# Kernel optimization log

Measured on AMD Instinct MI355X. Metric: run time of the kernel, lower is better.

## Reference

```python
import jax, jax.numpy as jnp
import numpy as np

D_MODEL = 1024
D_FF = 4096
N_HEADS = 16
D_HEAD = D_MODEL // N_HEADS
BSZ, SEQ = 2, 2048
EPS = 1e-6


def layer_norm(x, lam, beta):
    # torch impl: (x - mu) / (std_biased + eps) * lambda + beta
    mu = jnp.mean(x, axis=-1, keepdims=True)
    sigma = jnp.sqrt(jnp.mean((x - mu) ** 2, axis=-1, keepdims=True)) + EPS
    return (x - mu) / sigma * lam + beta


def setup_inputs() -> dict:
    key = jax.random.key(0)
    ks = jax.random.split(key, 10)
    s = 0.02
    x = jax.random.normal(ks[0], (BSZ, SEQ, D_MODEL), dtype=jnp.float32)
    mask = jnp.ones((BSZ, 1, 1, SEQ), dtype=jnp.int32)
    # nn.Linear weights stored [out, in]; y = x @ W.T
    Wq = jax.random.normal(ks[1], (D_MODEL, D_MODEL), dtype=jnp.float32) * s
    Wk = jax.random.normal(ks[2], (D_MODEL, D_MODEL), dtype=jnp.float32) * s
    Wv = jax.random.normal(ks[3], (D_MODEL, D_MODEL), dtype=jnp.float32) * s
    Wo = jax.random.normal(ks[4], (D_MODEL, D_MODEL), dtype=jnp.float32) * s
    w1 = jax.random.normal(ks[5], (D_FF, D_MODEL), dtype=jnp.float32) * s
    b1 = jnp.zeros((D_FF,), dtype=jnp.float32)
    w2 = jax.random.normal(ks[6], (D_MODEL, D_FF), dtype=jnp.float32) * s
    b2 = jnp.zeros((D_MODEL,), dtype=jnp.float32)
    g1 = jnp.ones((D_MODEL,), dtype=jnp.float32)
    be1 = jnp.zeros((D_MODEL,), dtype=jnp.float32)
    g2 = jnp.ones((D_MODEL,), dtype=jnp.float32)
    be2 = jnp.zeros((D_MODEL,), dtype=jnp.float32)
    return {"x": x, "mask": mask, "Wq": Wq, "Wk": Wk, "Wv": Wv, "Wo": Wo,
            "w1": w1, "b1": b1, "w2": w2, "b2": b2,
            "g1": g1, "be1": be1, "g2": g2, "be2": be2}


def reference(x, mask, Wq, Wk, Wv, Wo, w1, b1, w2, b2, g1, be1, g2, be2):
    b, s, _ = x.shape
    # projections (y = x @ W.T), split heads -> [b, h, s, dh]
    def split_heads(t):
        return t.reshape(b, s, N_HEADS, D_HEAD).transpose(0, 2, 1, 3)
    Q = split_heads(x @ Wq.T)
    K = split_heads(x @ Wk.T)
    V = split_heads(x @ Wv.T)
    score = jnp.einsum('bhqd,bhkd->bhqk', Q, K) / jnp.sqrt(jnp.float32(D_HEAD))
    score = jnp.where(mask == 0, -jnp.inf, score)
    attn = jax.nn.softmax(score, axis=-1)
    out = jnp.einsum('bhqk,bhkd->bhqd', attn, V)
    out = out.transpose(0, 2, 1, 3).reshape(b, s, D_MODEL)
    x1 = out @ Wo.T
    x2 = layer_norm(x1 + x, g1, be1)
    x3 = jax.nn.relu(x2 @ w1.T + b1) @ w2.T + b2
    x4 = layer_norm(x2 + x3, g2, be2)
    return x4
```

## Files before the change

kernel.cpp:

```cpp
#include <hip/hip_runtime.h>
#include <math.h>

typedef __attribute__((ext_vector_type(8))) short bf16x8;
typedef __attribute__((ext_vector_type(4))) float f32x4;
typedef __attribute__((ext_vector_type(8))) unsigned short us8;
typedef unsigned short u16;
typedef unsigned int u32;

constexpr int BSZ = 2, SEQ = 2048, DM = 1024, DFF = 4096, NH = 16, DH = 64;
constexpr int MROWS = BSZ * SEQ;

__device__ __forceinline__ float bf2f(u16 u) {
  union { unsigned int i; float f; } v; v.i = ((unsigned int)u) << 16; return v.f;
}
__device__ __forceinline__ u16 f2bf(float f) {
  union { float f; unsigned int i; } v; v.f = f;
  unsigned int r = v.i + 0x7fffu + ((v.i >> 16) & 1u);
  return (u16)(r >> 16);
}

#define GLOAD16(gp, lp) __builtin_amdgcn_global_load_lds( \
    (const __attribute__((address_space(1))) void*)(gp),  \
    (__attribute__((address_space(3))) void*)(lp), 16, 0, 0)
#define GLOAD4(gp, lp) __builtin_amdgcn_global_load_lds( \
    (const __attribute__((address_space(1))) void*)(gp),  \
    (__attribute__((address_space(3))) void*)(lp), 4, 0, 0)

__global__ __launch_bounds__(256) void cvt_all(
    const float* __restrict__ x, const float* __restrict__ Wq,
    const float* __restrict__ Wk, const float* __restrict__ Wv,
    const float* __restrict__ Wo, const float* __restrict__ w1,
    const float* __restrict__ w2, u16* __restrict__ xb,
    u16* __restrict__ Wqkvb, u16* __restrict__ Wob,
    u16* __restrict__ w1b, u16* __restrict__ w2b) {
  constexpr int M1 = 1 << 20;
  const int i = (blockIdx.x * 256 + threadIdx.x) * 8;
  const float* src;
  u16* dst;
  int off;
  if (i < 4 * M1)        { src = x;  dst = xb;            off = i;           }
  else if (i < 5 * M1)   { src = Wq; dst = Wqkvb;         off = i - 4 * M1;  }
  else if (i < 6 * M1)   { src = Wk; dst = Wqkvb + M1;    off = i - 5 * M1;  }
  else if (i < 7 * M1)   { src = Wv; dst = Wqkvb + 2 * M1; off = i - 6 * M1; }
  else if (i < 8 * M1)   { src = Wo; dst = Wob;           off = i - 7 * M1;  }
  else if (i < 12 * M1)  { src = w1; dst = w1b;           off = i - 8 * M1;  }
  else                   { src = w2; dst = w2b;           off = i - 12 * M1; }
  const float4 a = *(const float4*)(src + off);
  const float4 b = *(const float4*)(src + off + 4);
  uint4 o;
  o.x = f2bf(a.x) | ((unsigned)f2bf(a.y) << 16);
  o.y = f2bf(a.z) | ((unsigned)f2bf(a.w) << 16);
  o.z = f2bf(b.x) | ((unsigned)f2bf(b.y) << 16);
  o.w = f2bf(b.z) | ((unsigned)f2bf(b.w) << 16);
  *(uint4*)(dst + off) = o;
}

template <int BM, int BN, bool BIAS, bool RELU, bool OBF16>
__global__ __launch_bounds__(256) void gemm_bf16(
    const u16* __restrict__ A, const u16* __restrict__ B,
    const float* __restrict__ bias, float* __restrict__ Cf,
    u16* __restrict__ Cb, int M, int N, int K) {
  constexpr int MI = BM / 32, NI = BN / 32;
  __shared__ u16 As[2][BM * 32];
  __shared__ u16 Bs[2][BN * 32];
  const int tid = threadIdx.x;
  const int lane = tid & 63, wid = tid >> 6;

  const int nwg = gridDim.x * gridDim.y;
  int id = blockIdx.y * gridDim.x + blockIdx.x;
  id = (id & 7) * (nwg >> 3) + (id >> 3);
  const int bx = id % gridDim.x, by = id / gridDim.x;

  const int row0 = by * BM, col0 = bx * BN;
  const int wr = (wid >> 1) * (BM / 2), wc = (wid & 1) * (BN / 2);
  const int fr = lane & 15, hi = lane >> 4;

  f32x4 acc[MI][NI];
#pragma unroll
  for (int i = 0; i < MI; ++i)
#pragma unroll
    for (int j = 0; j < NI; ++j) acc[i][j] = {0.f, 0.f, 0.f, 0.f};

  const int sr = tid >> 2;
  const int se = (tid & 3) * 8;

#define STAGE(buf, k0)                                                        \
  {                                                                           \
    _Pragma("unroll")                                                         \
    for (int c = 0; c < BM * 64; c += 4096) {                                 \
      const int r = (c >> 6) + sr;                                            \
      GLOAD16(A + (size_t)(row0 + r) * K + ((k0) + se),                       \
              ((char*)As[buf]) + c + tid * 16);                               \
    }                                                                         \
    _Pragma("unroll")                                                         \
    for (int c = 0; c < BN * 64; c += 4096) {                                 \
      const int r = (c >> 6) + sr;                                            \
      GLOAD16(B + (size_t)(col0 + r) * K + ((k0) + se),                       \
              ((char*)Bs[buf]) + c + tid * 16);                               \
    }                                                                         \
  }

  STAGE(0, 0);
  __syncthreads();

  const int NIT = K / 32;
  for (int it = 0; it < NIT; ++it) {
    const int cur = it & 1;
    if (it + 1 < NIT) STAGE(cur ^ 1, (it + 1) * 32);

    bf16x8 af[MI], bv[NI];
#pragma unroll
    for (int mi = 0; mi < MI; ++mi)
      af[mi] = *(const bf16x8*)&As[cur][(wr + mi * 16 + fr) * 32 + hi * 8];
#pragma unroll
    for (int ni = 0; ni < NI; ++ni)
      bv[ni] = *(const bf16x8*)&Bs[cur][(wc + ni * 16 + fr) * 32 + hi * 8];
#pragma unroll
    for (int mi = 0; mi < MI; ++mi)
#pragma unroll
      for (int ni = 0; ni < NI; ++ni)
        acc[mi][ni] = __builtin_amdgcn_mfma_f32_16x16x32_bf16(
            af[mi], bv[ni], acc[mi][ni], 0, 0, 0);
    __syncthreads();
  }
#undef STAGE

  const int erow = row0 + wr + (hi << 2);
  const int ecol0 = col0 + wc;
#pragma unroll
  for (int ni = 0; ni < NI; ++ni) {
    const int col = ecol0 + ni * 16 + fr;
    const float bvv = BIAS ? bias[col] : 0.f;
#pragma unroll
    for (int mi = 0; mi < MI; ++mi) {
      const int rbase = erow + mi * 16;
#pragma unroll
      for (int j = 0; j < 4; ++j) {
        float v = acc[mi][ni][j] + bvv;
        if (RELU) v = fmaxf(v, 0.f);
        const size_t idx = (size_t)(rbase + j) * N + col;
        if (OBF16) Cb[idx] = f2bf(v); else Cf[idx] = v;
      }
    }
  }
}

__global__ __launch_bounds__(512) void attn_mfma(
    const u16* __restrict__ QKV, const int* __restrict__ mask,
    u16* __restrict__ Ob) {
  constexpr int KB = 64, QB = 128, NT = SEQ / KB;
  __shared__ u16 Kl[2][KB * 64];
  __shared__ u16 Vt[2][64 * KB];
  __shared__ int ml[2][KB];

  const int tid = threadIdx.x;
  const int lane = tid & 63, wid = tid >> 6;
  const int q0 = blockIdx.x * QB;
  const int bh = blockIdx.y;
  const int b = bh >> 4, h = bh & 15;
  const size_t base = (size_t)b * SEQ * 3072;
  const int fr = lane & 15, g = lane >> 4;

  const u16* qp = QKV + base + (size_t)(q0 + wid * 16 + fr) * 3072 + h * 64 + g * 8;
  bf16x8 qf0, qf1;
  {
    const float QSC = 0.18033688f;
    const us8 ua = *(const us8*)qp;
    const us8 ub = *(const us8*)(qp + 32);
    u32 pa[4], pb[4];
#pragma unroll
    for (int i = 0; i < 4; ++i) {
      const float a0 = bf2f(ua[2 * i]) * QSC, a1 = bf2f(ua[2 * i + 1]) * QSC;
      const float b0 = bf2f(ub[2 * i]) * QSC, b1 = bf2f(ub[2 * i + 1]) * QSC;
      asm("v_cvt_pk_bf16_f32 %0, %1, %2" : "=v"(pa[i]) : "v"(a0), "v"(a1));
      asm("v_cvt_pk_bf16_f32 %0, %1, %2" : "=v"(pb[i]) : "v"(b0), "v"(b1));
    }
    union { u32 d[4]; bf16x8 v; } c0, c1;
#pragma unroll
    for (int i = 0; i < 4; ++i) { c0.d[i] = pa[i]; c1.d[i] = pb[i]; }
    qf0 = c0.v; qf1 = c1.v;
  }

  const int krow = wid * 8 + (lane >> 3);
  const int kcol = 8 * ((lane & 7) ^ (lane >> 3));
  const u16* ksrc = QKV + base + 1024 + h * 64 + kcol;
  const int kdst = wid * 1024 + lane * 16;

  const int va = (tid & 255) >> 3;
  const int vq = tid & 7;
  const u16* vsrc = QKV + base + 2048 + h * 64 + vq * 8;
  const bool vstage = (wid < 4);

  f32x4 o[4] = {{0.f,0.f,0.f,0.f},{0.f,0.f,0.f,0.f},{0.f,0.f,0.f,0.f},{0.f,0.f,0.f,0.f}};
  float mreg = -3e38f, lreg = 0.f;

  {
    GLOAD16(ksrc + (size_t)krow * 3072, (char*)Kl[0] + kdst);
    if (wid == 4) GLOAD4(mask + b * SEQ + lane, (char*)ml[0] + lane * 4);
    if (vstage) {
      const us8 v0 = *(const us8*)(vsrc + (size_t)(2 * va) * 3072);
      const us8 v1 = *(const us8*)(vsrc + (size_t)(2 * va + 1) * 3072);
      char* vb = (char*)Vt[0];
#pragma unroll
      for (int i = 0; i < 8; ++i) {
        const int d = vq * 8 + i;
        const u32 wv = (u32)(u16)v0[i] | ((u32)(u16)v1[i] << 16);
        *(u32*)(vb + d * 128 + ((4 * va) ^ ((vq ^ i) << 4))) = wv;
      }
    }
  }
  __syncthreads();

  for (int it = 0; it < NT; ++it) {
    const int cur = it & 1, nxt = cur ^ 1;
    const int ktn = (it + 1) * KB;
    const bool pre = (it + 1 < NT);
    us8 v0 = {}, v1 = {};
    if (pre) {
      GLOAD16(ksrc + (size_t)(ktn + krow) * 3072, (char*)Kl[nxt] + kdst);
      if (wid == 4) GLOAD4(mask + b * SEQ + ktn + lane, (char*)ml[nxt] + lane * 4);
      if (vstage) {
        v0 = *(const us8*)(vsrc + (size_t)(ktn + 2 * va) * 3072);
        v1 = *(const us8*)(vsrc + (size_t)(ktn + 2 * va + 1) * 3072);
      }
    }

    f32x4 s[4];
#pragma unroll
    for (int t16 = 0; t16 < 4; ++t16) {
      const int kr = t16 * 16 + fr;
      const char* krp = (const char*)Kl[cur] + kr * 128;
      const int sw = (kr & 7) << 4;
      const bf16x8 kf0 = *(const bf16x8*)(krp + ((g * 16) ^ sw));
      const bf16x8 kf1 = *(const bf16x8*)(krp + ((g * 16 + 64) ^ sw));
      f32x4 a = {0.f, 0.f, 0.f, 0.f};
      a = __builtin_amdgcn_mfma_f32_16x16x32_bf16(kf0, qf0, a, 0, 0, 0);
      a = __builtin_amdgcn_mfma_f32_16x16x32_bf16(kf1, qf1, a, 0, 0, 0);
      s[t16] = a;
    }

#pragma unroll
    for (int t16 = 0; t16 < 4; ++t16) {
      const int4 mv = *(const int4*)&ml[cur][t16 * 16 + g * 4];
      const int* mp = (const int*)&mv;
#pragma unroll
      for (int j = 0; j < 4; ++j)
        if (mp[j] == 0) s[t16][j] = -3e38f;
    }

    float rmax = s[0][0];
#pragma unroll
    for (int t16 = 0; t16 < 4; ++t16)
#pragma unroll
      for (int j = 0; j < 4; ++j) rmax = fmaxf(rmax, s[t16][j]);

    if (!__all(rmax <= mreg + 12.f)) {
      rmax = fmaxf(rmax, __shfl_xor(rmax, 16));
      rmax = fmaxf(rmax, __shfl_xor(rmax, 32));
      const float mn = fmaxf(mreg, rmax);
      float sc;
      asm("v_exp_f32 %0, %1" : "=v"(sc) : "v"(mreg - mn));
      mreg = mn;
      lreg *= sc;
#pragma unroll
      for (int j = 0; j < 4; ++j) {
        const float scj = __shfl(sc, (g << 4) + g * 4 + j);
#pragma unroll
        for (int dt = 0; dt < 4; ++dt) o[dt][j] *= scj;
      }
    }

    float p[4][4];
#pragma unroll
    for (int t16 = 0; t16 < 4; ++t16)
#pragma unroll
      for (int j = 0; j < 4; ++j) {
        float e;
        asm("v_exp_f32 %0, %1" : "=v"(e) : "v"(s[t16][j] - mreg));
        p[t16][j] = e;
        lreg += e;
      }

    u32 plo[4], phi[4];
#pragma unroll
    for (int t16 = 0; t16 < 4; ++t16) {
      asm("v_cvt_pk_bf16_f32 %0, %1, %2"
          : "=v"(plo[t16]) : "v"(p[t16][0]), "v"(p[t16][1]));
      asm("v_cvt_pk_bf16_f32 %0, %1, %2"
          : "=v"(phi[t16]) : "v"(p[t16][2]), "v"(p[t16][3]));
    }

#pragma unroll
    for (int kh = 0; kh < 2; ++kh) {
      u32 fd[4];
#pragma unroll
      for (int hf = 0; hf < 2; ++hf) {
        const int sl = fr + ((((g & 1) << 1) + hf) << 4);
        const u32 c0l = (u32)__shfl((int)plo[kh * 2], sl);
        const u32 c0h = (u32)__shfl((int)phi[kh * 2], sl);
        const u32 c1l = (u32)__shfl((int)plo[kh * 2 + 1], sl);
        const u32 c1h = (u32)__shfl((int)phi[kh * 2 + 1], sl);
        const bool s1 = ((g >> 1) & 1) != 0;
        fd[hf * 2] = s1 ? c1l : c0l;
        fd[hf * 2 + 1] = s1 ? c1h : c0h;
      }
      union { u32 d[4]; bf16x8 v; } uu;
      uu.d[0] = fd[0]; uu.d[1] = fd[1]; uu.d[2] = fd[2]; uu.d[3] = fd[3];
      const bf16x8 pf = uu.v;
#pragma unroll
      for (int dt = 0; dt < 4; ++dt) {
        const int d = dt * 16 + fr;
        const int xd = (((d >> 3) ^ d) & 7) << 4;
        const bf16x8 vf = *(const bf16x8*)((const char*)Vt[cur] + d * 128 +
                                           ((g * 16 + kh * 64) ^ xd));
        o[dt] = __builtin_amdgcn_mfma_f32_16x16x32_bf16(pf, vf, o[dt], 0, 0, 0);
      }
    }

    if (pre && vstage) {
      char* vb = (char*)Vt[nxt];
#pragma unroll
      for (int i = 0; i < 8; ++i) {
        const int d = vq * 8 + i;
        const u32 wv = (u32)(u16)v0[i] | ((u32)(u16)v1[i] << 16);
        *(u32*)(vb + d * 128 + ((4 * va) ^ ((vq ^ i) << 4))) = wv;
      }
    }
    __syncthreads();
  }

  lreg += __shfl_xor(lreg, 16);
  lreg += __shfl_xor(lreg, 32);
  const float inv = 1.f / lreg;
#pragma unroll
  for (int j = 0; j < 4; ++j) {
    const float invj = __shfl(inv, (g << 4) + g * 4 + j);
    const int qrow = q0 + wid * 16 + g * 4 + j;
    u16* orow = Ob + (size_t)(b * SEQ + qrow) * DM + h * 64;
#pragma unroll
    for (int dt = 0; dt < 4; ++dt)
      orow[dt * 16 + fr] = f2bf(o[dt][j] * invj);
  }
}

template <bool ABF, bool BBF, bool OBF>
__global__ __launch_bounds__(256) void ln_add(const void* __restrict__ Ap,
                                              const void* __restrict__ Bp,
                                              const float* __restrict__ g,
                                              const float* __restrict__ be,
                                              void* __restrict__ outp) {
  __shared__ float red[2][4];
  __shared__ float mu_s, sig_s;
  const int row = blockIdx.x;
  const int tid = threadIdx.x;

  float4 a, b;
  if (ABF) {
    const ushort4 u = *(const ushort4*)((const u16*)Ap + (size_t)row * DM + tid * 4);
    a = make_float4(bf2f(u.x), bf2f(u.y), bf2f(u.z), bf2f(u.w));
  } else {
    a = *(const float4*)((const float*)Ap + (size_t)row * DM + tid * 4);
  }
  if (BBF) {
    const ushort4 u = *(const ushort4*)((const u16*)Bp + (size_t)row * DM + tid * 4);
    b = make_float4(bf2f(u.x), bf2f(u.y), bf2f(u.z), bf2f(u.w));
  } else {
    b = *(const float4*)((const float*)Bp + (size_t)row * DM + tid * 4);
  }
  float4 s = make_float4(a.x + b.x, a.y + b.y, a.z + b.z, a.w + b.w);

  float sum = s.x + s.y + s.z + s.w;
  float sq = s.x * s.x + s.y * s.y + s.z * s.z + s.w * s.w;
#pragma unroll
  for (int off = 32; off >= 1; off >>= 1) {
    sum += __shfl_xor(sum, off);
    sq += __shfl_xor(sq, off);
  }
  const int wid = tid >> 6;
  if ((tid & 63) == 0) { red[0][wid] = sum; red[1][wid] = sq; }
  __syncthreads();
  if (tid == 0) {
    float ts = red[0][0] + red[0][1] + red[0][2] + red[0][3];
    float tq = red[1][0] + red[1][1] + red[1][2] + red[1][3];
    float mu = ts * (1.f / DM);
    float var = tq * (1.f / DM) - mu * mu;
    mu_s = mu;
    sig_s = sqrtf(fmaxf(var, 0.f)) + 1e-6f;
  }
  __syncthreads();
  const float mu = mu_s, inv = 1.f / sig_s;
  const float4 gv = *(const float4*)(g + tid * 4);
  const float4 bv = *(const float4*)(be + tid * 4);
  float4 o;
  o.x = (s.x - mu) * inv * gv.x + bv.x;
  o.y = (s.y - mu) * inv * gv.y + bv.y;
  o.z = (s.z - mu) * inv * gv.z + bv.z;
  o.w = (s.w - mu) * inv * gv.w + bv.w;
  if (OBF) {
    u16* op = (u16*)outp + (size_t)row * DM + tid * 4;
    ushort4 o4;
    o4.x = f2bf(o.x); o4.y = f2bf(o.y); o4.z = f2bf(o.z); o4.w = f2bf(o.w);
    *(ushort4*)op = o4;
  } else {
    *(float4*)((float*)outp + (size_t)row * DM + tid * 4) = o;
  }
}

extern "C" void kernel_launch(void* const* d_in, const int* in_sizes, int n_in,
                              void* d_out, int out_size, void* d_ws,
                              size_t ws_size, hipStream_t stream) {
  const float* x  = (const float*)d_in[0];
  const int* mask = (const int*)d_in[1];
  const float* Wq = (const float*)d_in[2];
  const float* Wk = (const float*)d_in[3];
  const float* Wv = (const float*)d_in[4];
  const float* Wo = (const float*)d_in[5];
  const float* w1 = (const float*)d_in[6];
  const float* b1 = (const float*)d_in[7];
  const float* w2 = (const float*)d_in[8];
  const float* b2 = (const float*)d_in[9];
  const float* g1 = (const float*)d_in[10];
  const float* be1 = (const float*)d_in[11];
  const float* g2 = (const float*)d_in[12];
  const float* be2 = (const float*)d_in[13];
  float* out = (float*)d_out;
  float* ws = (float*)d_ws;

  u16*   QKVb  = (u16*)(ws + 0);
  u16*   xb    = (u16*)(ws + 6291456);
  u16*   Wqkvb = (u16*)(ws + 8388608);
  u16*   Wob   = (u16*)(ws + 9961472);
  u16*   w1b   = (u16*)(ws + 10485760);
  u16*   w2b   = (u16*)(ws + 12582912);
  u16*   Obf   = (u16*)(ws + 14680064);
  u16*   X1b   = (u16*)(ws + 16777216);
  u16*   X2b   = (u16*)(ws + 20971520);
  u16*   X3b   = (u16*)(ws + 23068672);
  u16*   Hb    = (u16*)(ws + 0);

  const dim3 blk(256);

  cvt_all<<<8192, blk, 0, stream>>>(x, Wq, Wk, Wv, Wo, w1, w2,
                                    xb, Wqkvb, Wob, w1b, w2b);

  gemm_bf16<128, 128, false, false, true><<<dim3(3072 / 128, MROWS / 128), blk, 0, stream>>>(
      xb, Wqkvb, nullptr, nullptr, QKVb, MROWS, 3072, DM);

  attn_mfma<<<dim3(SEQ / 128, BSZ * NH), dim3(512), 0, stream>>>(QKVb, mask, Obf);

  gemm_bf16<64, 128, false, false, true><<<dim3(DM / 128, MROWS / 64), blk, 0, stream>>>(
      Obf, Wob, nullptr, nullptr, X1b, MROWS, DM, DM);

  ln_add<true, true, true><<<dim3(MROWS), blk, 0, stream>>>(X1b, xb, g1, be1, X2b);

  gemm_bf16<128, 128, true, true, true><<<dim3(DFF / 128, MROWS / 128), blk, 0, stream>>>(
      X2b, w1b, b1, nullptr, Hb, MROWS, DFF, DM);

  gemm_bf16<64, 128, true, false, true><<<dim3(DM / 128, MROWS / 64), blk, 0, stream>>>(
      Hb, w2b, b2, nullptr, X3b, MROWS, DM, DFF);

  ln_add<true, true, false><<<dim3(MROWS), blk, 0, stream>>>(X2b, X3b, g2, be2, out);
}
```

Measured before the change: 272.3 us.

## Split-K the Wo and W2 GEMMs into two halves, summed in layernorm

```diff
diff --git a/kernel.cpp b/kernel.cpp
--- a/kernel.cpp
+++ b/kernel.cpp
@@ -55,11 +55,11 @@
   *(uint4*)(dst + off) = o;
 }
 
-template <int BM, int BN, bool BIAS, bool RELU, bool OBF16>
+template <int BM, int BN, bool BIAS, bool RELU>
 __global__ __launch_bounds__(256) void gemm_bf16(
     const u16* __restrict__ A, const u16* __restrict__ B,
-    const float* __restrict__ bias, float* __restrict__ Cf,
-    u16* __restrict__ Cb, int M, int N, int K) {
+    const float* __restrict__ bias, u16* __restrict__ Cb,
+    int M, int N, int K, int ld) {
   constexpr int MI = BM / 32, NI = BN / 32;
   __shared__ u16 As[2][BM * 32];
   __shared__ u16 Bs[2][BN * 32];
@@ -71,6 +71,10 @@
   id = (id & 7) * (nwg >> 3) + (id >> 3);
   const int bx = id % gridDim.x, by = id / gridDim.x;
 
+  const u16* Az = A + (size_t)blockIdx.z * K;
+  const u16* Bz = B + (size_t)blockIdx.z * K;
+  u16* Cz = Cb + (size_t)blockIdx.z * M * N;
+
   const int row0 = by * BM, col0 = bx * BN;
   const int wr = (wid >> 1) * (BM / 2), wc = (wid & 1) * (BN / 2);
   const int fr = lane & 15, hi = lane >> 4;
@@ -89,13 +93,13 @@
     _Pragma("unroll")                                                         \
     for (int c = 0; c < BM * 64; c += 4096) {                                 \
       const int r = (c >> 6) + sr;                                            \
-      GLOAD16(A + (size_t)(row0 + r) * K + ((k0) + se),                       \
+      GLOAD16(Az + (size_t)(row0 + r) * ld + ((k0) + se),                     \
               ((char*)As[buf]) + c + tid * 16);                               \
     }                                                                         \
     _Pragma("unroll")                                                         \
     for (int c = 0; c < BN * 64; c += 4096) {                                 \
       const int r = (c >> 6) + sr;                                            \
-      GLOAD16(B + (size_t)(col0 + r) * K + ((k0) + se),                       \
+      GLOAD16(Bz + (size_t)(col0 + r) * ld + ((k0) + se),                     \
               ((char*)Bs[buf]) + c + tid * 16);                               \
     }                                                                         \
   }
@@ -138,8 +142,7 @@
       for (int j = 0; j < 4; ++j) {
         float v = acc[mi][ni][j] + bvv;
         if (RELU) v = fmaxf(v, 0.f);
-        const size_t idx = (size_t)(rbase + j) * N + col;
-        if (OBF16) Cb[idx] = f2bf(v); else Cf[idx] = v;
+        Cz[(size_t)(rbase + j) * N + col] = f2bf(v);
       }
     }
   }
@@ -343,38 +346,37 @@
   }
 }
 
-template <bool ABF, bool BBF, bool OBF>
-__global__ __launch_bounds__(256) void ln_add(const void* __restrict__ Ap,
-                                              const void* __restrict__ Bp,
-                                              const float* __restrict__ g,
-                                              const float* __restrict__ be,
-                                              void* __restrict__ outp) {
+template <bool OBF, bool HASC, bool HASB>
+__global__ __launch_bounds__(256) void ln_add(
+    const u16* __restrict__ Ap, const u16* __restrict__ Bp,
+    const u16* __restrict__ Cp, const float* __restrict__ bias,
+    const float* __restrict__ g, const float* __restrict__ be,
+    void* __restrict__ outp) {
   __shared__ float red[2][4];
   __shared__ float mu_s, sig_s;
   const int row = blockIdx.x;
   const int tid = threadIdx.x;
-
-  float4 a, b;
-  if (ABF) {
-    const ushort4 u = *(const ushort4*)((const u16*)Ap + (size_t)row * DM + tid * 4);
-    a = make_float4(bf2f(u.x), bf2f(u.y), bf2f(u.z), bf2f(u.w));
-  } else {
-    a = *(const float4*)((const float*)Ap + (size_t)row * DM + tid * 4);
-  }
-  if (BBF) {
-    const ushort4 u = *(const ushort4*)((const u16*)Bp + (size_t)row * DM + tid * 4);
-    b = make_float4(bf2f(u.x), bf2f(u.y), bf2f(u.z), bf2f(u.w));
-  } else {
-    b = *(const float4*)((const float*)Bp + (size_t)row * DM + tid * 4);
-  }
-  float4 s = make_float4(a.x + b.x, a.y + b.y, a.z + b.z, a.w + b.w);
+  const size_t off = (size_t)row * DM + tid * 4;
+
+  const ushort4 ua = *(const ushort4*)(Ap + off);
+  const ushort4 ub = *(const ushort4*)(Bp + off);
+  float4 s = make_float4(bf2f(ua.x) + bf2f(ub.x), bf2f(ua.y) + bf2f(ub.y),
+                         bf2f(ua.z) + bf2f(ub.z), bf2f(ua.w) + bf2f(ub.w));
+  if (HASC) {
+    const ushort4 uc = *(const ushort4*)(Cp + off);
+    s.x += bf2f(uc.x); s.y += bf2f(uc.y); s.z += bf2f(uc.z); s.w += bf2f(uc.w);
+  }
+  if (HASB) {
+    const float4 bb = *(const float4*)(bias + tid * 4);
+    s.x += bb.x; s.y += bb.y; s.z += bb.z; s.w += bb.w;
+  }
 
   float sum = s.x + s.y + s.z + s.w;
   float sq = s.x * s.x + s.y * s.y + s.z * s.z + s.w * s.w;
 #pragma unroll
-  for (int off = 32; off >= 1; off >>= 1) {
-    sum += __shfl_xor(sum, off);
-    sq += __shfl_xor(sq, off);
+  for (int off2 = 32; off2 >= 1; off2 >>= 1) {
+    sum += __shfl_xor(sum, off2);
+    sq += __shfl_xor(sq, off2);
   }
   const int wid = tid >> 6;
   if ((tid & 63) == 0) { red[0][wid] = sum; red[1][wid] = sq; }
@@ -397,12 +399,12 @@
   o.z = (s.z - mu) * inv * gv.z + bv.z;
   o.w = (s.w - mu) * inv * gv.w + bv.w;
   if (OBF) {
-    u16* op = (u16*)outp + (size_t)row * DM + tid * 4;
+    u16* op = (u16*)outp + off;
     ushort4 o4;
     o4.x = f2bf(o.x); o4.y = f2bf(o.y); o4.z = f2bf(o.z); o4.w = f2bf(o.w);
     *(ushort4*)op = o4;
   } else {
-    *(float4*)((float*)outp + (size_t)row * DM + tid * 4) = o;
+    *(float4*)((float*)outp + off) = o;
   }
 }
 
@@ -433,9 +435,11 @@
   u16*   w1b   = (u16*)(ws + 10485760);
   u16*   w2b   = (u16*)(ws + 12582912);
   u16*   Obf   = (u16*)(ws + 14680064);
-  u16*   X1b   = (u16*)(ws + 16777216);
+  u16*   X1a   = (u16*)(ws + 16777216);
+  u16*   X1c   = (u16*)(ws + 18874368);
   u16*   X2b   = (u16*)(ws + 20971520);
-  u16*   X3b   = (u16*)(ws + 23068672);
+  u16*   X3a   = (u16*)(ws + 23068672);
+  u16*   X3c   = (u16*)(ws + 25165824);
   u16*   Hb    = (u16*)(ws + 0);
 
   const dim3 blk(256);
@@ -443,21 +447,23 @@
   cvt_all<<<8192, blk, 0, stream>>>(x, Wq, Wk, Wv, Wo, w1, w2,
                                     xb, Wqkvb, Wob, w1b, w2b);
 
-  gemm_bf16<128, 128, false, false, true><<<dim3(3072 / 128, MROWS / 128), blk, 0, stream>>>(
-      xb, Wqkvb, nullptr, nullptr, QKVb, MROWS, 3072, DM);
+  gemm_bf16<128, 128, false, false><<<dim3(3072 / 128, MROWS / 128), blk, 0, stream>>>(
+      xb, Wqkvb, nullptr, QKVb, MROWS, 3072, DM, DM);
 
   attn_mfma<<<dim3(SEQ / 128, BSZ * NH), dim3(512), 0, stream>>>(QKVb, mask, Obf);
 
-  gemm_bf16<64, 128, false, false, true><<<dim3(DM / 128, MROWS / 64), blk, 0, stream>>>(
-      Obf, Wob, nullptr, nullptr, X1b, MROWS, DM, DM);
-
-  ln_add<true, true, true><<<dim3(MROWS), blk, 0, stream>>>(X1b, xb, g1, be1, X2b);
-
-  gemm_bf16<128, 128, true, true, true><<<dim3(DFF / 128, MROWS / 128), blk, 0, stream>>>(
-      X2b, w1b, b1, nullptr, Hb, MROWS, DFF, DM);
-
-  gemm_bf16<64, 128, true, false, true><<<dim3(DM / 128, MROWS / 64), blk, 0, stream>>>(
-      Hb, w2b, b2, nullptr, X3b, MROWS, DM, DFF);
-
-  ln_add<true, true, false><<<dim3(MROWS), blk, 0, stream>>>(X2b, X3b, g2, be2, out);
-}
+  gemm_bf16<64, 128, false, false><<<dim3(DM / 128, MROWS / 64, 2), blk, 0, stream>>>(
+      Obf, Wob, nullptr, X1a, MROWS, DM, DM / 2, DM);
+
+  ln_add<true, true, false><<<dim3(MROWS), blk, 0, stream>>>(
+      X1a, xb, X1c, nullptr, g1, be1, X2b);
+
+  gemm_bf16<128, 128, true, true><<<dim3(DFF / 128, MROWS / 128), blk, 0, stream>>>(
+      X2b, w1b, b1, Hb, MROWS, DFF, DM, DM);
+
+  gemm_bf16<64, 128, false, false><<<dim3(DM / 128, MROWS / 64, 2), blk, 0, stream>>>(
+      Hb, w2b, nullptr, X3a, MROWS, DM, DFF / 2, DFF);
+
+  ln_add<false, true, true><<<dim3(MROWS), blk, 0, stream>>>(
+      X2b, X3a, X3c, b2, g2, be2, out);
+}
```

New measurement: 262.4 us (median of 2 runs). 1.04x faster.
